# Kernel optimization log

Hardware: AMD Instinct MI355X
Metric: run time of the kernel (lower is better)

The kernel has to match this reference:

```python
import jax, jax.numpy as jnp
import numpy as np
from functools import partial

FS = 30.0
CUTOFF = 3.3
ORDER = 5
PADLEN = 18  # scipy filtfilt default: 3 * max(len(a), len(b)) = 3 * 6


def butter_lowpass_np(order, Wn):
    """Digital Butterworth lowpass (b, a), matching scipy.signal.butter."""
    # analog prototype poles (buttap)
    m = np.arange(-order + 1, order, 2)
    p = -np.exp(1j * np.pi * m / (2 * order))
    k = 1.0
    # pre-warp frequency (scipy uses internal fs = 2.0)
    fs = 2.0
    warped = 2 * fs * np.tan(np.pi * Wn / fs)
    p = warped * p
    k = k * warped ** order
    # bilinear transform
    fs2 = 2 * fs
    p_z = (fs2 + p) / (fs2 - p)
    z_z = -np.ones(order)
    k_z = k * np.real(1.0 / np.prod(fs2 - p))
    b = k_z * np.real(np.poly(z_z))
    a = np.real(np.poly(p_z))
    return b.astype(np.float64), a.astype(np.float64)


def lfilter_zi_np(b, a):
    """Steady-state initial conditions, matching scipy.signal.lfilter_zi."""
    n = len(a)
    comp = np.zeros((n - 1, n - 1))
    comp[0, :] = -a[1:] / a[0]
    if n > 2:
        comp[1:, :-1] = np.eye(n - 2)
    B = b[1:] - a[1:] * b[0]
    return np.linalg.solve(np.eye(n - 1) - comp.T, B)


def lfilter(b, a, x, zi):
    """Direct-form II transposed IIR filter along a 1-D signal via lax.scan."""
    def step(z, xt):
        y = b[0] * xt + z[0]
        z_shift = jnp.concatenate([z[1:], jnp.zeros(1, z.dtype)])
        z_new = b[1:] * xt + z_shift - a[1:] * y
        return z_new, y
    _, y = jax.lax.scan(step, zi, x)
    return y


def filtfilt_1d(b, a, zi, x):
    """Zero-phase filtering with odd-extension padding (scipy filtfilt defaults)."""
    left = 2 * x[0] - x[PADLEN:0:-1]
    right = 2 * x[-1] - x[-2:-(PADLEN + 2):-1]
    ext = jnp.concatenate([left, x, right])
    y = lfilter(b, a, ext, zi * ext[0])
    y = lfilter(b, a, y[::-1], zi * y[-1])[::-1]
    return y[PADLEN:-PADLEN]


def setup_inputs() -> dict:
    key = jax.random.key(0)
    x = jax.random.normal(key, (4096, 8192), dtype=jnp.float32)
    Wn = CUTOFF / (FS / 2.0)
    b_np, a_np = butter_lowpass_np(ORDER, Wn)
    zi_np = lfilter_zi_np(b_np, a_np)
    return {
        "x": x,
        "b": jnp.asarray(b_np, dtype=jnp.float32),
        "a": jnp.asarray(a_np, dtype=jnp.float32),
        "zi": jnp.asarray(zi_np, dtype=jnp.float32),
    }


def reference(x, b, a, zi):
    # batched zero-phase Butterworth lowpass, [batch, length] -> [batch, length]
    return jax.vmap(partial(filtfilt_1d, b, a, zi))(x)
```

## Files before the change

### kernel.cpp

```cpp
#include <hip/hip_runtime.h>
#include <stdint.h>


#define NN   8192
#define PADL 18
#define LC   32
#define TPB  256

typedef uint32_t u32;

__device__ __forceinline__ void gload16(const float* g, float* l) {
    __builtin_amdgcn_global_load_lds(
        (const __attribute__((address_space(1))) u32*)g,
        (__attribute__((address_space(3))) u32*)l, 16, 0, 0);
}

__device__ __forceinline__ float SC(const float* lds, int c, int e) {
    return lds[(c << 5) + (((e >> 2) ^ (c & 7)) << 2) + (e & 3)];
}
__device__ __forceinline__ float4 LDQ(const float* lds, int c, int j) {
    return *reinterpret_cast<const float4*>(lds + (c << 5) + ((j ^ (c & 7)) << 2));
}
__device__ __forceinline__ void STQ(float* lds, int c, int j, float4 v) {
    *reinterpret_cast<float4*>(lds + (c << 5) + ((j ^ (c & 7)) << 2)) = v;
}

#define STEP(xv) do {                               \
    float y_ = fmaf(b0, (xv), z0);                  \
    z0 = fmaf(na1, y_, fmaf(b1, (xv), z1));         \
    z1 = fmaf(na2, y_, fmaf(b2, (xv), z2));         \
    z2 = fmaf(na3, y_, fmaf(b3, (xv), z3));         \
    z3 = fmaf(na4, y_, fmaf(b4, (xv), z4));         \
    z4 = fmaf(na5, y_, b5 * (xv));                  \
    yv = y_;                                        \
} while (0)

__global__ __launch_bounds__(TPB, 4) void GREEN_62869731278967_filtfilt(
    const float* __restrict__ x,
    const float* __restrict__ bc,
    const float* __restrict__ ac,
    const float* __restrict__ zc,
    float* __restrict__ out)
{
    __shared__ float lds[NN];
    const int row = blockIdx.x;
    const int tid = threadIdx.x;
    const float* xr   = x   + (size_t)row * NN;
    float*       outr = out + (size_t)row * NN;

    const float b0 = bc[0], b1 = bc[1], b2 = bc[2], b3 = bc[3], b4 = bc[4], b5 = bc[5];
    const float na1 = -ac[1], na2 = -ac[2], na3 = -ac[3], na4 = -ac[4], na5 = -ac[5];
    const float zi0 = zc[0], zi1 = zc[1], zi2 = zc[2], zi3 = zc[3], zi4 = zc[4];

    {
        const int wv = tid >> 6, L = tid & 63;
        const float* srow = xr + ((wv << 11) + ((L >> 3) << 5) + (((L & 7) ^ (L >> 3)) << 2));
        float* lbase = lds + (wv << 11);
#pragma unroll
        for (int k = 0; k < 8; ++k)
            gload16(srow + (k << 8), lbase + (k << 8));
    }
    asm volatile("s_waitcnt vmcnt(0)" ::: "memory");
    __syncthreads();

    float yreg[LC];
    float ytail[PADL];
    float z0, z1, z2, z3, z4, yv;

    if (tid == 0) {
        const float x0 = lds[0];
        float v0 = 2.f * x0 - lds[PADL];
        z0 = zi0 * v0; z1 = zi1 * v0; z2 = zi2 * v0; z3 = zi3 * v0; z4 = zi4 * v0;
#pragma unroll
        for (int t = 0; t < PADL; ++t) {
            float v = 2.f * x0 - lds[PADL - t];
            STEP(v);
        }
    } else {
        float v0 = SC(lds, tid - 1, 0);
        z0 = zi0 * v0; z1 = zi1 * v0; z2 = zi2 * v0; z3 = zi3 * v0; z4 = zi4 * v0;
#pragma unroll
        for (int j = 0; j < 8; ++j) {
            float4 q = LDQ(lds, tid - 1, j);
            STEP(q.x); STEP(q.y); STEP(q.z); STEP(q.w);
        }
    }
#pragma unroll
    for (int j = 0; j < 8; ++j) {
        float4 q = LDQ(lds, tid, j);
        STEP(q.x); yreg[4 * j + 0] = yv;
        STEP(q.y); yreg[4 * j + 1] = yv;
        STEP(q.z); yreg[4 * j + 2] = yv;
        STEP(q.w); yreg[4 * j + 3] = yv;
    }
    if (tid == TPB - 1) {
        const float xN = SC(lds, TPB - 1, 31);
#pragma unroll
        for (int i = 0; i < PADL; ++i) {
            float v = 2.f * xN - SC(lds, TPB - 1, 30 - i);
            STEP(v);
            ytail[i] = yv;
        }
    }
    __syncthreads();

#pragma unroll
    for (int j = 0; j < 8; ++j)
        STQ(lds, tid, j, make_float4(yreg[4 * j], yreg[4 * j + 1],
                                     yreg[4 * j + 2], yreg[4 * j + 3]));
    __syncthreads();

    if (tid == TPB - 1) {
        float u0 = ytail[PADL - 1];
        z0 = zi0 * u0; z1 = zi1 * u0; z2 = zi2 * u0; z3 = zi3 * u0; z4 = zi4 * u0;
#pragma unroll
        for (int s = 0; s < PADL; ++s) STEP(ytail[PADL - 1 - s]);
    } else {
        float u0 = SC(lds, tid + 1, LC - 1);
        z0 = zi0 * u0; z1 = zi1 * u0; z2 = zi2 * u0; z3 = zi3 * u0; z4 = zi4 * u0;
#pragma unroll
        for (int j = 7; j >= 0; --j) {
            float4 q = LDQ(lds, tid + 1, j);
            STEP(q.w); STEP(q.z); STEP(q.y); STEP(q.x);
        }
    }
#pragma unroll
    for (int i = 0; i < LC; ++i) { STEP(yreg[LC - 1 - i]); yreg[LC - 1 - i] = yv; }

#pragma unroll
    for (int q = 0; q < LC / 4; ++q) {
        float4 v;
        v.x = yreg[4 * q + 0];
        v.y = yreg[4 * q + 1];
        v.z = yreg[4 * q + 2];
        v.w = yreg[4 * q + 3];
        *reinterpret_cast<float4*>(outr + tid * LC + 4 * q) = v;
    }
}

extern "C" void kernel_launch(void* const* d_in, const int* in_sizes, int n_in,
                              void* d_out, int out_size, void* d_ws, size_t ws_size,
                              hipStream_t stream) {
    const float* x  = (const float*)d_in[0];
    const float* b  = (const float*)d_in[1];
    const float* a  = (const float*)d_in[2];
    const float* zi = (const float*)d_in[3];
    float* out = (float*)d_out;
    const int rows = in_sizes[0] / NN;
    GREEN_62869731278967_filtfilt<<<rows, TPB, 0, stream>>>(x, b, a, zi, out);
}
```

Measured before the change: 65.24 us.

## Process four rows per block with double-buffered async LDS prefetch

Each block now handles four rows and uses two LDS buffers, so the global-to-LDS load of the next row is issued while the current row is filtered. Explicit vmcnt waits and raw barriers replace __syncthreads. The aim is to hide global load latency behind the serial recurrence and to amortize block launch. In exchange, LDS per block doubles, so fewer blocks fit per CU (launch bounds drop to 2 waves-per-EU), and the grid has 1024 blocks instead of 4096. The code also assumes the row count is a multiple of four.

```diff
diff --git a/kernel.cpp b/kernel.cpp
--- a/kernel.cpp
+++ b/kernel.cpp
@@ -6,6 +6,7 @@
 #define PADL 18
 #define LC   32
 #define TPB  256
+#define ROWS 4
 
 typedef uint32_t u32;
 
@@ -15,14 +16,22 @@
         (__attribute__((address_space(3))) u32*)l, 16, 0, 0);
 }
 
-__device__ __forceinline__ float SC(const float* lds, int c, int e) {
-    return lds[(c << 5) + (((e >> 2) ^ (c & 7)) << 2) + (e & 3)];
+#define WAITV(N) do { asm volatile("s_waitcnt vmcnt(" #N ")" ::: "memory"); \
+                      __builtin_amdgcn_sched_barrier(0); } while (0)
+#define WAITL()  do { asm volatile("s_waitcnt lgkmcnt(0)" ::: "memory");    \
+                      __builtin_amdgcn_sched_barrier(0); } while (0)
+#define BAR()    do { __builtin_amdgcn_sched_barrier(0);                    \
+                      __builtin_amdgcn_s_barrier();                         \
+                      __builtin_amdgcn_sched_barrier(0); } while (0)
+
+__device__ __forceinline__ float SC(const float* b, int c, int e) {
+    return b[(c << 5) + (((e >> 2) ^ (c & 7)) << 2) + (e & 3)];
 }
-__device__ __forceinline__ float4 LDQ(const float* lds, int c, int j) {
-    return *reinterpret_cast<const float4*>(lds + (c << 5) + ((j ^ (c & 7)) << 2));
+__device__ __forceinline__ float4 LDQ(const float* b, int c, int j) {
+    return *reinterpret_cast<const float4*>(b + (c << 5) + ((j ^ (c & 7)) << 2));
 }
-__device__ __forceinline__ void STQ(float* lds, int c, int j, float4 v) {
-    *reinterpret_cast<float4*>(lds + (c << 5) + ((j ^ (c & 7)) << 2)) = v;
+__device__ __forceinline__ void STQ(float* b, int c, int j, float4 v) {
+    *reinterpret_cast<float4*>(b + (c << 5) + ((j ^ (c & 7)) << 2)) = v;
 }
 
 #define STEP(xv) do {                               \
@@ -35,106 +44,119 @@
     yv = y_;                                        \
 } while (0)
 
-__global__ __launch_bounds__(TPB, 4) void GREEN_62869731278967_filtfilt(
+__global__ __launch_bounds__(TPB, 2) void GREEN_62869731278967_filtfilt(
     const float* __restrict__ x,
     const float* __restrict__ bc,
     const float* __restrict__ ac,
     const float* __restrict__ zc,
     float* __restrict__ out)
 {
-    __shared__ float lds[NN];
-    const int row = blockIdx.x;
+    __shared__ float lds[2][NN];
     const int tid = threadIdx.x;
-    const float* xr   = x   + (size_t)row * NN;
-    float*       outr = out + (size_t)row * NN;
+    const int row0 = blockIdx.x * ROWS;
+    const int wv = tid >> 6, L = tid & 63;
 
     const float b0 = bc[0], b1 = bc[1], b2 = bc[2], b3 = bc[3], b4 = bc[4], b5 = bc[5];
     const float na1 = -ac[1], na2 = -ac[2], na3 = -ac[3], na4 = -ac[4], na5 = -ac[5];
     const float zi0 = zc[0], zi1 = zc[1], zi2 = zc[2], zi3 = zc[3], zi4 = zc[4];
 
-    {
-        const int wv = tid >> 6, L = tid & 63;
-        const float* srow = xr + ((wv << 11) + ((L >> 3) << 5) + (((L & 7) ^ (L >> 3)) << 2));
-        float* lbase = lds + (wv << 11);
+    const float* xlane = x + (size_t)row0 * NN
+                       + ((wv << 11) + ((L >> 3) << 5) + (((L & 7) ^ (L >> 3)) << 2));
+
 #pragma unroll
-        for (int k = 0; k < 8; ++k)
-            gload16(srow + (k << 8), lbase + (k << 8));
-    }
-    asm volatile("s_waitcnt vmcnt(0)" ::: "memory");
-    __syncthreads();
+    for (int k = 0; k < 8; ++k) gload16(xlane + (k << 8),            &lds[0][(wv << 11) + (k << 8)]);
+#pragma unroll
+    for (int k = 0; k < 8; ++k) gload16(xlane + NN + (k << 8),       &lds[1][(wv << 11) + (k << 8)]);
 
-    float yreg[LC];
-    float ytail[PADL];
-    float z0, z1, z2, z3, z4, yv;
+#pragma unroll
+    for (int r = 0; r < ROWS; ++r) {
+        float* B = lds[r & 1];
+        float* outr = out + (size_t)(row0 + r) * NN;
 
-    if (tid == 0) {
-        const float x0 = lds[0];
-        float v0 = 2.f * x0 - lds[PADL];
-        z0 = zi0 * v0; z1 = zi1 * v0; z2 = zi2 * v0; z3 = zi3 * v0; z4 = zi4 * v0;
+        if (r == 0 || r == ROWS - 1) WAITV(8); else WAITV(16);
+        BAR();
+
+        float yreg[LC];
+        float ytail[PADL];
+        float z0, z1, z2, z3, z4, yv;
+        if (tid == 0) {
+            const float x0 = B[0];
+            float v0 = 2.f * x0 - B[PADL];
+            z0 = zi0 * v0; z1 = zi1 * v0; z2 = zi2 * v0; z3 = zi3 * v0; z4 = zi4 * v0;
 #pragma unroll
-        for (int t = 0; t < PADL; ++t) {
-            float v = 2.f * x0 - lds[PADL - t];
-            STEP(v);
+            for (int t = 0; t < PADL; ++t) {
+                float v = 2.f * x0 - B[PADL - t];
+                STEP(v);
+            }
+        } else {
+            float v0 = SC(B, tid - 1, 0);
+            z0 = zi0 * v0; z1 = zi1 * v0; z2 = zi2 * v0; z3 = zi3 * v0; z4 = zi4 * v0;
+#pragma unroll
+            for (int j = 0; j < 8; ++j) {
+                float4 q = LDQ(B, tid - 1, j);
+                STEP(q.x); STEP(q.y); STEP(q.z); STEP(q.w);
+            }
         }
-    } else {
-        float v0 = SC(lds, tid - 1, 0);
-        z0 = zi0 * v0; z1 = zi1 * v0; z2 = zi2 * v0; z3 = zi3 * v0; z4 = zi4 * v0;
 #pragma unroll
         for (int j = 0; j < 8; ++j) {
-            float4 q = LDQ(lds, tid - 1, j);
-            STEP(q.x); STEP(q.y); STEP(q.z); STEP(q.w);
+            float4 q = LDQ(B, tid, j);
+            STEP(q.x); yreg[4 * j + 0] = yv;
+            STEP(q.y); yreg[4 * j + 1] = yv;
+            STEP(q.z); yreg[4 * j + 2] = yv;
+            STEP(q.w); yreg[4 * j + 3] = yv;
         }
-    }
+        if (tid == TPB - 1) {
+            const float xN = SC(B, TPB - 1, 31);
 #pragma unroll
-    for (int j = 0; j < 8; ++j) {
-        float4 q = LDQ(lds, tid, j);
-        STEP(q.x); yreg[4 * j + 0] = yv;
-        STEP(q.y); yreg[4 * j + 1] = yv;
-        STEP(q.z); yreg[4 * j + 2] = yv;
-        STEP(q.w); yreg[4 * j + 3] = yv;
-    }
-    if (tid == TPB - 1) {
-        const float xN = SC(lds, TPB - 1, 31);
-#pragma unroll
-        for (int i = 0; i < PADL; ++i) {
-            float v = 2.f * xN - SC(lds, TPB - 1, 30 - i);
-            STEP(v);
-            ytail[i] = yv;
+            for (int i = 0; i < PADL; ++i) {
+                float v = 2.f * xN - SC(B, TPB - 1, 30 - i);
+                STEP(v);
+                ytail[i] = yv;
+            }
         }
-    }
-    __syncthreads();
+        BAR();
 
 #pragma unroll
-    for (int j = 0; j < 8; ++j)
-        STQ(lds, tid, j, make_float4(yreg[4 * j], yreg[4 * j + 1],
-                                     yreg[4 * j + 2], yreg[4 * j + 3]));
-    __syncthreads();
+        for (int j = 0; j < 8; ++j)
+            STQ(B, tid, j, make_float4(yreg[4 * j], yreg[4 * j + 1],
+                                       yreg[4 * j + 2], yreg[4 * j + 3]));
+        WAITL();
+        BAR();
 
-    if (tid == TPB - 1) {
-        float u0 = ytail[PADL - 1];
-        z0 = zi0 * u0; z1 = zi1 * u0; z2 = zi2 * u0; z3 = zi3 * u0; z4 = zi4 * u0;
+        if (tid == TPB - 1) {
+            float u0 = ytail[PADL - 1];
+            z0 = zi0 * u0; z1 = zi1 * u0; z2 = zi2 * u0; z3 = zi3 * u0; z4 = zi4 * u0;
 #pragma unroll
-        for (int s = 0; s < PADL; ++s) STEP(ytail[PADL - 1 - s]);
-    } else {
-        float u0 = SC(lds, tid + 1, LC - 1);
-        z0 = zi0 * u0; z1 = zi1 * u0; z2 = zi2 * u0; z3 = zi3 * u0; z4 = zi4 * u0;
+            for (int s = 0; s < PADL; ++s) STEP(ytail[PADL - 1 - s]);
+        } else {
+            float u0 = SC(B, tid + 1, LC - 1);
+            z0 = zi0 * u0; z1 = zi1 * u0; z2 = zi2 * u0; z3 = zi3 * u0; z4 = zi4 * u0;
 #pragma unroll
-        for (int j = 7; j >= 0; --j) {
-            float4 q = LDQ(lds, tid + 1, j);
-            STEP(q.w); STEP(q.z); STEP(q.y); STEP(q.x);
+            for (int j = 7; j >= 0; --j) {
+                float4 q = LDQ(B, tid + 1, j);
+                STEP(q.w); STEP(q.z); STEP(q.y); STEP(q.x);
+            }
         }
-    }
 #pragma unroll
-    for (int i = 0; i < LC; ++i) { STEP(yreg[LC - 1 - i]); yreg[LC - 1 - i] = yv; }
+        for (int i = 0; i < LC; ++i) { STEP(yreg[LC - 1 - i]); yreg[LC - 1 - i] = yv; }
 
 #pragma unroll
-    for (int q = 0; q < LC / 4; ++q) {
-        float4 v;
-        v.x = yreg[4 * q + 0];
-        v.y = yreg[4 * q + 1];
-        v.z = yreg[4 * q + 2];
-        v.w = yreg[4 * q + 3];
-        *reinterpret_cast<float4*>(outr + tid * LC + 4 * q) = v;
+        for (int q = 0; q < LC / 4; ++q) {
+            float4 v;
+            v.x = yreg[4 * q + 0];
+            v.y = yreg[4 * q + 1];
+            v.z = yreg[4 * q + 2];
+            v.w = yreg[4 * q + 3];
+            *reinterpret_cast<float4*>(outr + tid * LC + 4 * q) = v;
+        }
+
+        if (r + 2 < ROWS) {
+            BAR();
+            const float* xn = xlane + (size_t)(r + 2) * NN;
+#pragma unroll
+            for (int k = 0; k < 8; ++k)
+                gload16(xn + (k << 8), &B[(wv << 11) + (k << 8)]);
+        }
     }
 }
 
@@ -147,5 +169,6 @@
     const float* zi = (const float*)d_in[3];
     float* out = (float*)d_out;
     const int rows = in_sizes[0] / NN;
-    GREEN_62869731278967_filtfilt<<<rows, TPB, 0, stream>>>(x, b, a, zi, out);
+    const int blocks = rows / ROWS;
+    GREEN_62869731278967_filtfilt<<<blocks, TPB, 0, stream>>>(x, b, a, zi, out);
 }
```

Measured after the change: 80.09 us. 22.8% more time.

## Double per-thread chunk length and shorten warm-up to half a chunk

Applied to the files above, without the earlier changes.

Each thread now filters 64 samples with 128 threads per row instead of 32 samples with 256 threads. The boundary-state warm-up still runs over 32 samples, taken from the tail (forward) or head (backward) of the neighbouring chunk, so total redundant recurrence work per row drops. The global-to-LDS direct loads are replaced by ordinary float4 loads followed by swizzled LDS stores, and the backward pass writes only the needed 32 forward outputs per chunk to LDS. The trade-off is a longer serial dependency chain per thread, more registers for the 64-entry buffer, and fewer waves in flight.

```diff
diff --git a/kernel.cpp b/kernel.cpp
--- a/kernel.cpp
+++ b/kernel.cpp
@@ -1,28 +1,19 @@
 #include <hip/hip_runtime.h>
-#include <stdint.h>
 
 
 #define NN   8192
 #define PADL 18
-#define LC   32
-#define TPB  256
+#define LC   64
+#define TPB  128
 
-typedef uint32_t u32;
-
-__device__ __forceinline__ void gload16(const float* g, float* l) {
-    __builtin_amdgcn_global_load_lds(
-        (const __attribute__((address_space(1))) u32*)g,
-        (__attribute__((address_space(3))) u32*)l, 16, 0, 0);
+__device__ __forceinline__ float4 LDQ(const float* b, int c, int j) {
+    return *reinterpret_cast<const float4*>(b + (c << 6) + ((j ^ (c & 15)) << 2));
 }
-
-__device__ __forceinline__ float SC(const float* lds, int c, int e) {
-    return lds[(c << 5) + (((e >> 2) ^ (c & 7)) << 2) + (e & 3)];
+__device__ __forceinline__ void STQ(float* b, int c, int j, float4 v) {
+    *reinterpret_cast<float4*>(b + (c << 6) + ((j ^ (c & 15)) << 2)) = v;
 }
-__device__ __forceinline__ float4 LDQ(const float* lds, int c, int j) {
-    return *reinterpret_cast<const float4*>(lds + (c << 5) + ((j ^ (c & 7)) << 2));
-}
-__device__ __forceinline__ void STQ(float* lds, int c, int j, float4 v) {
-    *reinterpret_cast<float4*>(lds + (c << 5) + ((j ^ (c & 7)) << 2)) = v;
+__device__ __forceinline__ float SC(const float* b, int c, int e) {
+    return b[(c << 6) + (((e >> 2) ^ (c & 15)) << 2) + (e & 3)];
 }
 
 #define STEP(xv) do {                               \
@@ -35,32 +26,27 @@
     yv = y_;                                        \
 } while (0)
 
-__global__ __launch_bounds__(TPB, 4) void GREEN_62869731278967_filtfilt(
+__global__ __launch_bounds__(TPB, 2) void GREEN_62869731278967_filtfilt(
     const float* __restrict__ x,
     const float* __restrict__ bc,
     const float* __restrict__ ac,
     const float* __restrict__ zc,
     float* __restrict__ out)
 {
-    __shared__ float lds[NN];
-    const int row = blockIdx.x;
+    __shared__ float B[NN];
     const int tid = threadIdx.x;
-    const float* xr   = x   + (size_t)row * NN;
-    float*       outr = out + (size_t)row * NN;
+    const float* xr   = x   + (size_t)blockIdx.x * NN;
+    float*       outr = out + (size_t)blockIdx.x * NN;
 
     const float b0 = bc[0], b1 = bc[1], b2 = bc[2], b3 = bc[3], b4 = bc[4], b5 = bc[5];
     const float na1 = -ac[1], na2 = -ac[2], na3 = -ac[3], na4 = -ac[4], na5 = -ac[5];
     const float zi0 = zc[0], zi1 = zc[1], zi2 = zc[2], zi3 = zc[3], zi4 = zc[4];
 
-    {
-        const int wv = tid >> 6, L = tid & 63;
-        const float* srow = xr + ((wv << 11) + ((L >> 3) << 5) + (((L & 7) ^ (L >> 3)) << 2));
-        float* lbase = lds + (wv << 11);
 #pragma unroll
-        for (int k = 0; k < 8; ++k)
-            gload16(srow + (k << 8), lbase + (k << 8));
+    for (int q = 0; q < 16; ++q) {
+        float4 v = *reinterpret_cast<const float4*>(xr + (q << 9) + (tid << 2));
+        STQ(B, (q << 3) + (tid >> 4), tid & 15, v);
     }
-    asm volatile("s_waitcnt vmcnt(0)" ::: "memory");
     __syncthreads();
 
     float yreg[LC];
@@ -68,36 +54,38 @@
     float z0, z1, z2, z3, z4, yv;
 
     if (tid == 0) {
-        const float x0 = lds[0];
-        float v0 = 2.f * x0 - lds[PADL];
+        const float x0 = B[0];
+        float v0 = 2.f * x0 - B[PADL];
         z0 = zi0 * v0; z1 = zi1 * v0; z2 = zi2 * v0; z3 = zi3 * v0; z4 = zi4 * v0;
 #pragma unroll
         for (int t = 0; t < PADL; ++t) {
-            float v = 2.f * x0 - lds[PADL - t];
+            float v = 2.f * x0 - B[PADL - t];
             STEP(v);
         }
     } else {
-        float v0 = SC(lds, tid - 1, 0);
-        z0 = zi0 * v0; z1 = zi1 * v0; z2 = zi2 * v0; z3 = zi3 * v0; z4 = zi4 * v0;
+        const int cp = tid - 1;
+        float4 q8 = LDQ(B, cp, 8);
+        z0 = zi0 * q8.x; z1 = zi1 * q8.x; z2 = zi2 * q8.x; z3 = zi3 * q8.x; z4 = zi4 * q8.x;
+        STEP(q8.x); STEP(q8.y); STEP(q8.z); STEP(q8.w);
 #pragma unroll
-        for (int j = 0; j < 8; ++j) {
-            float4 q = LDQ(lds, tid - 1, j);
+        for (int j = 9; j < 16; ++j) {
+            float4 q = LDQ(B, cp, j);
             STEP(q.x); STEP(q.y); STEP(q.z); STEP(q.w);
         }
     }
 #pragma unroll
-    for (int j = 0; j < 8; ++j) {
-        float4 q = LDQ(lds, tid, j);
+    for (int j = 0; j < 16; ++j) {
+        float4 q = LDQ(B, tid, j);
         STEP(q.x); yreg[4 * j + 0] = yv;
         STEP(q.y); yreg[4 * j + 1] = yv;
         STEP(q.z); yreg[4 * j + 2] = yv;
         STEP(q.w); yreg[4 * j + 3] = yv;
     }
     if (tid == TPB - 1) {
-        const float xN = SC(lds, TPB - 1, 31);
+        const float xN = SC(B, TPB - 1, 63);
 #pragma unroll
         for (int i = 0; i < PADL; ++i) {
-            float v = 2.f * xN - SC(lds, TPB - 1, 30 - i);
+            float v = 2.f * xN - SC(B, TPB - 1, 62 - i);
             STEP(v);
             ytail[i] = yv;
         }
@@ -106,8 +94,8 @@
 
 #pragma unroll
     for (int j = 0; j < 8; ++j)
-        STQ(lds, tid, j, make_float4(yreg[4 * j], yreg[4 * j + 1],
-                                     yreg[4 * j + 2], yreg[4 * j + 3]));
+        STQ(B, tid, j, make_float4(yreg[4 * j], yreg[4 * j + 1],
+                                   yreg[4 * j + 2], yreg[4 * j + 3]));
     __syncthreads();
 
     if (tid == TPB - 1) {
@@ -116,25 +104,32 @@
 #pragma unroll
         for (int s = 0; s < PADL; ++s) STEP(ytail[PADL - 1 - s]);
     } else {
-        float u0 = SC(lds, tid + 1, LC - 1);
-        z0 = zi0 * u0; z1 = zi1 * u0; z2 = zi2 * u0; z3 = zi3 * u0; z4 = zi4 * u0;
+        const int cn = tid + 1;
+        float4 q7 = LDQ(B, cn, 7);
+        z0 = zi0 * q7.w; z1 = zi1 * q7.w; z2 = zi2 * q7.w; z3 = zi3 * q7.w; z4 = zi4 * q7.w;
+        STEP(q7.w); STEP(q7.z); STEP(q7.y); STEP(q7.x);
 #pragma unroll
-        for (int j = 7; j >= 0; --j) {
-            float4 q = LDQ(lds, tid + 1, j);
+        for (int j = 6; j >= 0; --j) {
+            float4 q = LDQ(B, cn, j);
             STEP(q.w); STEP(q.z); STEP(q.y); STEP(q.x);
         }
     }
 #pragma unroll
-    for (int i = 0; i < LC; ++i) { STEP(yreg[LC - 1 - i]); yreg[LC - 1 - i] = yv; }
+    for (int j = 15; j >= 0; --j) {
+        STEP(yreg[4 * j + 3]); yreg[4 * j + 3] = yv;
+        STEP(yreg[4 * j + 2]); yreg[4 * j + 2] = yv;
+        STEP(yreg[4 * j + 1]); yreg[4 * j + 1] = yv;
+        STEP(yreg[4 * j + 0]); yreg[4 * j + 0] = yv;
+    }
 
 #pragma unroll
-    for (int q = 0; q < LC / 4; ++q) {
+    for (int k = 0; k < 16; ++k) {
         float4 v;
-        v.x = yreg[4 * q + 0];
-        v.y = yreg[4 * q + 1];
-        v.z = yreg[4 * q + 2];
-        v.w = yreg[4 * q + 3];
-        *reinterpret_cast<float4*>(outr + tid * LC + 4 * q) = v;
+        v.x = yreg[4 * k + 0];
+        v.y = yreg[4 * k + 1];
+        v.z = yreg[4 * k + 2];
+        v.w = yreg[4 * k + 3];
+        *reinterpret_cast<float4*>(outr + (tid << 6) + (k << 2)) = v;
     }
 }
 
```

After: 72.99 us. 11.9% more time.
